# Kernel optimization log

Hardware: AMD Instinct MI355X
Metric: run time of the kernel (lower is better)

## Reference

```python
import jax, jax.numpy as jnp
import numpy as np

BATCH, T, N_STATE, N_IN, N_OUT = 256, 4096, 32, 8, 8
DT = 1e-3


def setup_inputs() -> dict:
    key = jax.random.key(0)
    k_u, k_x0, k_A, k_B, k_C, k_D = jax.random.split(key, 6)
    t = jnp.arange(T, dtype=jnp.float32) * DT
    u = jax.random.normal(k_u, (BATCH, T, N_IN), dtype=jnp.float32)
    x0 = jax.random.normal(k_x0, (BATCH, N_STATE), dtype=jnp.float32)
    # Stable-ish LTI system parameters
    A = (0.1 / np.sqrt(N_STATE)) * jax.random.normal(k_A, (N_STATE, N_STATE), dtype=jnp.float32) - 0.5 * jnp.eye(N_STATE, dtype=jnp.float32)
    B = jax.random.normal(k_B, (N_STATE, N_IN), dtype=jnp.float32) / np.sqrt(N_IN)
    C = jax.random.normal(k_C, (N_OUT, N_STATE), dtype=jnp.float32) / np.sqrt(N_STATE)
    D = jax.random.normal(k_D, (N_OUT, N_IN), dtype=jnp.float32) / np.sqrt(N_IN)
    return {"t": t, "u": u, "x0": x0, "A": A, "B": B, "C": C, "D": D}


def _dopri5_solve(t, u, x0, A, B):
    """Fixed-step Dopri5 (Dormand-Prince 5th order) on a uniform grid.

    Mirrors diffrax.diffeqsolve(Dopri5, ConstantStepSize, dt0=t[1], saveat=ts=t):
    one RK step per grid interval. u is evaluated at stage times via linear
    interpolation between grid samples.
    """
    dt = t[1] - t[0]

    def f(x, uu):  # vector field: dx = A x + B u
        return x @ A.T + uu @ B.T

    ut = jnp.swapaxes(u, 0, 1)  # [T, BATCH, N_IN]

    def step(x, uu):
        u0, u1 = uu
        du = u1 - u0
        k1 = f(x, u0)
        k2 = f(x + dt * (0.2 * k1), u0 + 0.2 * du)
        k3 = f(x + dt * (3.0 / 40.0 * k1 + 9.0 / 40.0 * k2), u0 + 0.3 * du)
        k4 = f(x + dt * (44.0 / 45.0 * k1 - 56.0 / 15.0 * k2 + 32.0 / 9.0 * k3), u0 + 0.8 * du)
        k5 = f(x + dt * (19372.0 / 6561.0 * k1 - 25360.0 / 2187.0 * k2 + 64448.0 / 6561.0 * k3 - 212.0 / 729.0 * k4), u0 + (8.0 / 9.0) * du)
        k6 = f(x + dt * (9017.0 / 3168.0 * k1 - 355.0 / 33.0 * k2 + 46732.0 / 5247.0 * k3 + 49.0 / 176.0 * k4 - 5103.0 / 18656.0 * k5), u1)
        xn = x + dt * (35.0 / 384.0 * k1 + 500.0 / 1113.0 * k3 + 125.0 / 192.0 * k4 - 2187.0 / 6784.0 * k5 + 11.0 / 84.0 * k6)
        return xn, xn

    _, xs_rest = jax.lax.scan(step, x0, (ut[:-1], ut[1:]))
    xs = jnp.concatenate([x0[None], xs_rest], axis=0)  # [T, BATCH, N_STATE]
    return jnp.swapaxes(xs, 0, 1)  # [BATCH, T, N_STATE]


def reference(t, u, x0, A, B, C, D):
    xs = _dopri5_solve(t, u, x0, A, B)          # state trajectory [BATCH, T, N_STATE]
    ys = xs @ C.T + u @ D.T                      # output y = C x + D u, [BATCH, T, N_OUT]
    return xs, ys
```

## Files before the change

### kernel.cpp

```cpp
#include <hip/hip_runtime.h>

#define BATCH 256
#define TT 4096
#define NS 32
#define NI 8
#define NO 8
#define LCH 64
#define NCHUNKS 64

#define WS_M  0
#define WS_N0 1024
#define WS_N1 1280
#define WS_ML 1536
#define WS_V  2560
#define WS_S  (2560 + BATCH * NCHUNKS * NS)
#define WS_F  (WS_S + BATCH * NCHUNKS * NS)

__device__ __forceinline__ float dot4(float4 a, float4 b) {
    return a.x * b.x + a.y * b.y + a.z * b.z + a.w * b.w;
}
__device__ __forceinline__ float4 ld4(const float* p) { return *(const float4*)p; }

__global__ __launch_bounds__(256) void k_pre(const float* __restrict__ tarr,
                                             const float* __restrict__ A,
                                             const float* __restrict__ B,
                                             float* __restrict__ ws) {
    __shared__ float sA[NS * NS], sB[NS * NI];
    __shared__ float Ka[6][NS * NS];
    __shared__ float Kb[6][NS * NI];
    __shared__ float Kc[6][NS * NI];
    __shared__ float Sa[NS * NS], Sb[NS * NI], Sc[NS * NI];
    __shared__ float Pq[2][NS * NS];
    __shared__ float Ms[NS * NS];

    const int tid = threadIdx.x;
    const float dt = tarr[1] - tarr[0];

    for (int e = tid; e < NS * NS; e += 256) sA[e] = A[e];
    for (int e = tid; e < NS * NI; e += 256) sB[e] = B[e];
    __syncthreads();
    for (int e = tid; e < NS * NS; e += 256) Ka[0][e] = sA[e];
    for (int e = tid; e < NS * NI; e += 256) { Kb[0][e] = sB[e]; Kc[0][e] = 0.f; }
    __syncthreads();

    const float atab[5][5] = {
        {0.2f, 0.f, 0.f, 0.f, 0.f},
        {3.f / 40.f, 9.f / 40.f, 0.f, 0.f, 0.f},
        {44.f / 45.f, -56.f / 15.f, 32.f / 9.f, 0.f, 0.f},
        {19372.f / 6561.f, -25360.f / 2187.f, 64448.f / 6561.f, -212.f / 729.f, 0.f},
        {9017.f / 3168.f, -355.f / 33.f, 46732.f / 5247.f, 49.f / 176.f, -5103.f / 18656.f}};
    const float ctab[6] = {0.f, 0.2f, 0.3f, 0.8f, 8.f / 9.f, 1.f};

    for (int st = 1; st <= 5; ++st) {
        for (int e = tid; e < NS * NS; e += 256) {
            float acc = 0.f;
            for (int j = 0; j < st; ++j) acc += atab[st - 1][j] * Ka[j][e];
            Sa[e] = acc;
        }
        for (int e = tid; e < NS * NI; e += 256) {
            float ab = 0.f, ac = 0.f;
            for (int j = 0; j < st; ++j) {
                ab += atab[st - 1][j] * Kb[j][e];
                ac += atab[st - 1][j] * Kc[j][e];
            }
            Sb[e] = ab; Sc[e] = ac;
        }
        __syncthreads();
        {
            const int j = tid & 31, ig = tid >> 5;
            for (int r = 0; r < 4; ++r) {
                const int row = ig + 8 * r;
                float acc = 0.f;
                for (int k = 0; k < NS; ++k) acc += sA[row * NS + k] * Sa[k * NS + j];
                Ka[st][row * NS + j] = sA[row * NS + j] + dt * acc;
            }
            const int jb = tid & 7, rb = tid >> 3;
            float ab = 0.f, ac = 0.f;
            for (int k = 0; k < NS; ++k) {
                ab += sA[rb * NS + k] * Sb[k * NI + jb];
                ac += sA[rb * NS + k] * Sc[k * NI + jb];
            }
            Kb[st][rb * NI + jb] = sB[rb * NI + jb] + dt * ab;
            Kc[st][rb * NI + jb] = ctab[st] * sB[rb * NI + jb] + dt * ac;
        }
        __syncthreads();
    }

    const float btab[6] = {35.f / 384.f, 0.f, 500.f / 1113.f, 125.f / 192.f,
                           -2187.f / 6784.f, 11.f / 84.f};
    for (int e = tid; e < NS * NS; e += 256) {
        float acc = 0.f;
        for (int i2 = 0; i2 < 6; ++i2) acc += btab[i2] * Ka[i2][e];
        const float m = dt * acc + (((e / NS) == (e % NS)) ? 1.f : 0.f);
        ws[WS_M + e] = m;
        Pq[0][e] = m;
        Ms[e] = m;
    }
    for (int e = tid; e < NS * NI; e += 256) {
        float ap = 0.f, aq = 0.f;
        for (int i2 = 0; i2 < 6; ++i2) {
            ap += btab[i2] * Kb[i2][e];
            aq += btab[i2] * Kc[i2][e];
        }
        const float P = dt * ap, Q = dt * aq;
        ws[WS_N0 + e] = P - Q;
        ws[WS_N1 + e] = Q;
        Sb[e] = P - Q;
        Sc[e] = Q;
    }
    __syncthreads();

    int cur = 0;
    for (int itq = 0; itq < 6; ++itq) {
        const int j = tid & 31, ig = tid >> 5;
        for (int r = 0; r < 4; ++r) {
            const int row = ig + 8 * r;
            float acc = 0.f;
            for (int k = 0; k < NS; ++k) acc += Pq[cur][row * NS + k] * Pq[cur][k * NS + j];
            Pq[cur ^ 1][row * NS + j] = acc;
        }
        __syncthreads();
        cur ^= 1;
        if (itq == 2)
            for (int e = tid; e < NS * NS; e += 256) Sa[e] = Pq[cur][e];
    }
    for (int e = tid; e < NS * NS; e += 256) ws[WS_ML + e] = Pq[cur][e];

    float* cb = &Ka[0][0];
    const int rr = tid >> 3, mm = tid & 7;

    float mrow[NS], m8row[NS];
#pragma unroll
    for (int kk = 0; kk < NS; ++kk) { mrow[kk] = Ms[rr * NS + kk]; m8row[kk] = Sa[rr * NS + kk]; }

    {
        float acc = 0.f;
#pragma unroll
        for (int kk = 0; kk < NS; ++kk) acc += mrow[kk] * Sc[kk * NI + mm];
        const float h = Sb[tid] + acc;
        cb[tid] = h;
        ws[WS_F + 63 * (NS * NI) + tid] = h;
    }
    __syncthreads();
    for (int i = 1; i < 8; ++i) {
        float acc = 0.f;
#pragma unroll
        for (int kk = 0; kk < NS; ++kk) acc += m8row[kk] * cb[(i - 1) * 256 + kk * NI + mm];
        cb[i * 256 + tid] = acc;
        ws[WS_F + (63 - 8 * i) * (NS * NI) + tid] = acc;
        __syncthreads();
    }
    int pp = 0;
    for (int k = 1; k < 8; ++k) {
        float acc[8];
#pragma unroll
        for (int i = 0; i < 8; ++i) {
            float a = 0.f;
#pragma unroll
            for (int kk = 0; kk < NS; ++kk) a += mrow[kk] * cb[pp * 2048 + i * 256 + kk * NI + mm];
            acc[i] = a;
        }
#pragma unroll
        for (int i = 0; i < 8; ++i) {
            cb[(pp ^ 1) * 2048 + i * 256 + tid] = acc[i];
            ws[WS_F + (63 - 8 * i - k) * (NS * NI) + tid] = acc[i];
        }
        __syncthreads();
        pp ^= 1;
    }
    ws[WS_F + 64 * (NS * NI) + tid] = Sc[tid];
}

__global__ __launch_bounds__(256, 2) void k_phase1(const float* __restrict__ u,
                                                   float* __restrict__ ws) {
    __shared__ float4 sF[64 * 64];

    const int tid = threadIdx.x;

    const float4* Fg = (const float4*)(ws + WS_F);
    for (int idx = tid; idx < 64 * 64; idx += 256) {
        const int j = idx >> 6, q = (idx >> 3) & 7, s = idx & 7;
        sF[idx] = Fg[(j << 6) + (s << 3) + q];
    }
    __syncthreads();

    const int task = blockIdx.x * 4 + (tid >> 6);
    const int c = task % (NCHUNKS - 1), g = task / (NCHUNKS - 1);
    const int l = tid & 63;
    const int beta = l >> 3, s8 = l & 7;
    const int b = g * 8 + beta;
    const int t0 = c * LCH;
    const float* ub = u + ((size_t)b * TT + t0) * NI;

    float4 ua = ld4(ub), uc = ld4(ub + 4);
    float a0 = 0.f, a1 = 0.f, a2 = 0.f, a3 = 0.f;

#pragma unroll 4
    for (int j = 0; j < 64; ++j) {
        const float4 na = ld4(ub + (j + 1) * NI);
        const float4 nb = ld4(ub + (j + 1) * NI + 4);
        const float4* fj = &sF[(j << 6) + s8];
        const float4 f0 = fj[0], f1 = fj[8], f2 = fj[16], f3 = fj[24];
        const float4 f4 = fj[32], f5 = fj[40], f6 = fj[48], f7 = fj[56];
        a0 += dot4(f0, ua) + dot4(f1, uc);
        a1 += dot4(f2, ua) + dot4(f3, uc);
        a2 += dot4(f4, ua) + dot4(f5, uc);
        a3 += dot4(f6, ua) + dot4(f7, uc);
        ua = na; uc = nb;
    }

    const float* Ft = ws + WS_F + 64 * (NS * NI) + 32 * s8;
    a0 += dot4(ld4(Ft), ua) + dot4(ld4(Ft + 4), uc);
    a1 += dot4(ld4(Ft + 8), ua) + dot4(ld4(Ft + 12), uc);
    a2 += dot4(ld4(Ft + 16), ua) + dot4(ld4(Ft + 20), uc);
    a3 += dot4(ld4(Ft + 24), ua) + dot4(ld4(Ft + 28), uc);

    *(float4*)(ws + WS_V + ((size_t)b * NCHUNKS + c) * NS + 4 * s8) =
        make_float4(a0, a1, a2, a3);
}

__global__ __launch_bounds__(64) void k_phase2(const float* __restrict__ x0,
                                               float* __restrict__ ws) {
    const float* ML = ws + WS_ML;
    const float* v = ws + WS_V;
    float* sst = ws + WS_S;
    const int b = blockIdx.x;
    const int l = threadIdx.x, i = l & 31, h = l >> 5;

    float mlr[16];
#pragma unroll
    for (int jj = 0; jj < 16; ++jj) mlr[jj] = ML[i * NS + 16 * h + jj];

    float x = x0[b * NS + i];
    for (int c = 0; c < NCHUNKS; ++c) {
        if (h == 0) sst[((size_t)b * NCHUNKS + c) * NS + i] = x;
        if (c == NCHUNKS - 1) break;
        float p = 0.f;
#pragma unroll
        for (int jj = 0; jj < 16; ++jj) p += mlr[jj] * __shfl(x, 16 * h + jj, 64);
        p += __shfl_xor(p, 32, 64);
        x = p + v[((size_t)b * NCHUNKS + c) * NS + i];
    }
}

__global__ __launch_bounds__(64, 1) void k_phase3(const float* __restrict__ u,
                                                  float* __restrict__ ws,
                                                  float* __restrict__ out,
                                                  const float* __restrict__ Cc,
                                                  const float* __restrict__ Dd) {
    const float* M = ws + WS_M;
    const float* N0 = ws + WS_N0;
    const float* N1 = ws + WS_N1;

    const int task = blockIdx.x;
    const int c = task % NCHUNKS, g = task / NCHUNKS;
    const int l = threadIdx.x;
    const int beta = l >> 3, s8 = l & 7;
    const int b = g * 8 + beta;

    float4 mq[4][8];
#pragma unroll
    for (int r = 0; r < 4; ++r)
#pragma unroll
        for (int jj = 0; jj < 8; ++jj) mq[r][jj] = ld4(M + (4 * s8 + r) * NS + 4 * jj);

    float4 n0q[4][2], n1q[4][2];
#pragma unroll
    for (int r = 0; r < 4; ++r) {
        n0q[r][0] = ld4(N0 + (4 * s8 + r) * NI);
        n0q[r][1] = ld4(N0 + (4 * s8 + r) * NI + 4);
        n1q[r][0] = ld4(N1 + (4 * s8 + r) * NI);
        n1q[r][1] = ld4(N1 + (4 * s8 + r) * NI + 4);
    }

    float4 cq[8], dq[2];
#pragma unroll
    for (int jj = 0; jj < 8; ++jj) cq[jj] = ld4(Cc + s8 * NS + 4 * jj);
    dq[0] = ld4(Dd + s8 * NI);
    dq[1] = ld4(Dd + s8 * NI + 4);

    __shared__ float4 xb[2][8 * 9];

    const int t0 = c * LCH;
    const float* ub = u + (size_t)b * TT * NI;
    float4 u0a = ld4(ub + t0 * NI), u0b = ld4(ub + t0 * NI + 4);
    float4 u1a = ld4(ub + (t0 + 1) * NI), u1b = ld4(ub + (t0 + 1) * NI + 4);

    float4 mine = ld4(ws + WS_S + ((size_t)b * NCHUNKS + c) * NS + 4 * s8);
    xb[0][beta * 9 + s8] = mine;
    asm volatile("s_waitcnt lgkmcnt(0)" ::: "memory");
    __builtin_amdgcn_sched_barrier(0);

    float* yout = out + (size_t)BATCH * TT * NS;
    int cur = 0;
    for (int js = 0; js < LCH; ++js) {
        const int t = t0 + js;
        float4 xq[8];
#pragma unroll
        for (int jj = 0; jj < 8; ++jj) xq[jj] = xb[cur][beta * 9 + jj];

        const int tp = (t + 2 < TT - 1) ? (t + 2) : (TT - 1);
        const float4 u2a = ld4(ub + tp * NI);
        const float4 u2b = ld4(ub + tp * NI + 4);

        *(float4*)(out + ((size_t)b * TT + t) * NS + 4 * s8) = mine;
        float yv = 0.f;
#pragma unroll
        for (int jj = 0; jj < 8; ++jj) yv += dot4(cq[jj], xq[jj]);
        yv += dot4(dq[0], u0a) + dot4(dq[1], u0b);
        yout[((size_t)b * TT + t) * NO + s8] = yv;

        if (js < LCH - 1) {
            float w0 = dot4(n0q[0][0], u0a) + dot4(n0q[0][1], u0b) + dot4(n1q[0][0], u1a) + dot4(n1q[0][1], u1b);
            float w1 = dot4(n0q[1][0], u0a) + dot4(n0q[1][1], u0b) + dot4(n1q[1][0], u1a) + dot4(n1q[1][1], u1b);
            float w2 = dot4(n0q[2][0], u0a) + dot4(n0q[2][1], u0b) + dot4(n1q[2][0], u1a) + dot4(n1q[2][1], u1b);
            float w3 = dot4(n0q[3][0], u0a) + dot4(n0q[3][1], u0b) + dot4(n1q[3][0], u1a) + dot4(n1q[3][1], u1b);
#pragma unroll
            for (int jj = 0; jj < 8; ++jj) {
                const float4 xv = xq[jj];
                w0 += dot4(mq[0][jj], xv);
                w1 += dot4(mq[1][jj], xv);
                w2 += dot4(mq[2][jj], xv);
                w3 += dot4(mq[3][jj], xv);
            }
            mine = make_float4(w0, w1, w2, w3);
            xb[cur ^ 1][beta * 9 + s8] = mine;
            u0a = u1a; u0b = u1b;
            u1a = u2a; u1b = u2b;
        }
        asm volatile("s_waitcnt lgkmcnt(0)" ::: "memory");
        __builtin_amdgcn_sched_barrier(0);
        cur ^= 1;
    }
}

extern "C" void kernel_launch(void* const* d_in, const int* in_sizes, int n_in,
                              void* d_out, int out_size, void* d_ws, size_t ws_size,
                              hipStream_t stream) {
    const float* t = (const float*)d_in[0];
    const float* u = (const float*)d_in[1];
    const float* x0 = (const float*)d_in[2];
    const float* A = (const float*)d_in[3];
    const float* B = (const float*)d_in[4];
    const float* C = (const float*)d_in[5];
    const float* D = (const float*)d_in[6];
    float* out = (float*)d_out;
    float* ws = (float*)d_ws;

    k_pre<<<dim3(1), dim3(256), 0, stream>>>(t, A, B, ws);
    k_phase1<<<dim3(8 * (NCHUNKS - 1)), dim3(256), 0, stream>>>(u, ws);
    k_phase2<<<dim3(BATCH), dim3(64), 0, stream>>>(x0, ws);
    k_phase3<<<dim3(32 * NCHUNKS), dim3(64), 0, stream>>>(u, ws, out, C, D);
}
```

Baseline: 342.0 us.

## Replace LDS state exchange with wavefront shuffles in phase-3 recurrence

The per-step state broadcast in k_phase3 used to go through a double-buffered shared-memory array with explicit lgkmcnt waits and scheduling barriers. It now uses cross-lane __shfl reads inside the single 64-lane wavefront. The change also splits the dot-product accumulations into independent partial sums to shorten dependency chains, and switches to incrementing pointers for the x, y and u accesses. Shuffles on AMD still go through the LDS crossbar (ds_bpermute), so each step now does 32 shuffles instead of 8 float4 LDS reads, which may cost as much as it saves.

```diff
diff --git a/kernel.cpp b/kernel.cpp
--- a/kernel.cpp
+++ b/kernel.cpp
@@ -257,6 +257,7 @@
     const int l = threadIdx.x;
     const int beta = l >> 3, s8 = l & 7;
     const int b = g * 8 + beta;
+    const int src_base = l & 56;
 
     float4 mq[4][8];
 #pragma unroll
@@ -279,58 +280,61 @@
     dq[0] = ld4(Dd + s8 * NI);
     dq[1] = ld4(Dd + s8 * NI + 4);
 
-    __shared__ float4 xb[2][8 * 9];
-
     const int t0 = c * LCH;
     const float* ub = u + (size_t)b * TT * NI;
-    float4 u0a = ld4(ub + t0 * NI), u0b = ld4(ub + t0 * NI + 4);
-    float4 u1a = ld4(ub + (t0 + 1) * NI), u1b = ld4(ub + (t0 + 1) * NI + 4);
+    const float* u_last = ub + (size_t)(TT - 1) * NI;
+    const float* up = ub + (size_t)t0 * NI;
+    float4 u0a = ld4(up), u0b = ld4(up + 4);
+    float4 u1a = ld4(up + NI), u1b = ld4(up + NI + 4);
+    const float* up2 = up + 2 * NI;
 
     float4 mine = ld4(ws + WS_S + ((size_t)b * NCHUNKS + c) * NS + 4 * s8);
-    xb[0][beta * 9 + s8] = mine;
-    asm volatile("s_waitcnt lgkmcnt(0)" ::: "memory");
-    __builtin_amdgcn_sched_barrier(0);
-
-    float* yout = out + (size_t)BATCH * TT * NS;
-    int cur = 0;
+
+    float* xp = out + ((size_t)b * TT + t0) * NS + 4 * s8;
+    float* yp = out + (size_t)BATCH * TT * NS + ((size_t)b * TT + t0) * NO + s8;
+
     for (int js = 0; js < LCH; ++js) {
-        const int t = t0 + js;
         float4 xq[8];
 #pragma unroll
-        for (int jj = 0; jj < 8; ++jj) xq[jj] = xb[cur][beta * 9 + jj];
-
-        const int tp = (t + 2 < TT - 1) ? (t + 2) : (TT - 1);
-        const float4 u2a = ld4(ub + tp * NI);
-        const float4 u2b = ld4(ub + tp * NI + 4);
-
-        *(float4*)(out + ((size_t)b * TT + t) * NS + 4 * s8) = mine;
-        float yv = 0.f;
-#pragma unroll
-        for (int jj = 0; jj < 8; ++jj) yv += dot4(cq[jj], xq[jj]);
-        yv += dot4(dq[0], u0a) + dot4(dq[1], u0b);
-        yout[((size_t)b * TT + t) * NO + s8] = yv;
+        for (int jj = 0; jj < 8; ++jj) {
+            xq[jj].x = __shfl(mine.x, src_base + jj, 64);
+            xq[jj].y = __shfl(mine.y, src_base + jj, 64);
+            xq[jj].z = __shfl(mine.z, src_base + jj, 64);
+            xq[jj].w = __shfl(mine.w, src_base + jj, 64);
+        }
+
+        const float* uq = (up2 > u_last) ? u_last : up2;
+        const float4 u2a = ld4(uq);
+        const float4 u2b = ld4(uq + 4);
+
+        *(float4*)xp = mine;
+
+        float ya = dot4(cq[0], xq[0]) + dot4(cq[1], xq[1]) + dot4(cq[2], xq[2]) + dot4(cq[3], xq[3]);
+        float yb = dot4(cq[4], xq[4]) + dot4(cq[5], xq[5]) + dot4(cq[6], xq[6]) + dot4(cq[7], xq[7]);
+        ya += dot4(dq[0], u0a);
+        yb += dot4(dq[1], u0b);
+        *yp = ya + yb;
 
         if (js < LCH - 1) {
-            float w0 = dot4(n0q[0][0], u0a) + dot4(n0q[0][1], u0b) + dot4(n1q[0][0], u1a) + dot4(n1q[0][1], u1b);
-            float w1 = dot4(n0q[1][0], u0a) + dot4(n0q[1][1], u0b) + dot4(n1q[1][0], u1a) + dot4(n1q[1][1], u1b);
-            float w2 = dot4(n0q[2][0], u0a) + dot4(n0q[2][1], u0b) + dot4(n1q[2][0], u1a) + dot4(n1q[2][1], u1b);
-            float w3 = dot4(n0q[3][0], u0a) + dot4(n0q[3][1], u0b) + dot4(n1q[3][0], u1a) + dot4(n1q[3][1], u1b);
-#pragma unroll
-            for (int jj = 0; jj < 8; ++jj) {
-                const float4 xv = xq[jj];
-                w0 += dot4(mq[0][jj], xv);
-                w1 += dot4(mq[1][jj], xv);
-                w2 += dot4(mq[2][jj], xv);
-                w3 += dot4(mq[3][jj], xv);
+            float w0, w1, w2, w3;
+#pragma unroll
+            for (int r = 0; r < 4; ++r) {
+                const float pn = dot4(n0q[r][0], u0a) + dot4(n0q[r][1], u0b) +
+                                 dot4(n1q[r][0], u1a) + dot4(n1q[r][1], u1b);
+                const float pe = dot4(mq[r][0], xq[0]) + dot4(mq[r][2], xq[2]) +
+                                 dot4(mq[r][4], xq[4]) + dot4(mq[r][6], xq[6]);
+                const float po = dot4(mq[r][1], xq[1]) + dot4(mq[r][3], xq[3]) +
+                                 dot4(mq[r][5], xq[5]) + dot4(mq[r][7], xq[7]);
+                const float w = pn + pe + po;
+                if (r == 0) w0 = w; else if (r == 1) w1 = w; else if (r == 2) w2 = w; else w3 = w;
             }
             mine = make_float4(w0, w1, w2, w3);
-            xb[cur ^ 1][beta * 9 + s8] = mine;
             u0a = u1a; u0b = u1b;
             u1a = u2a; u1b = u2b;
         }
-        asm volatile("s_waitcnt lgkmcnt(0)" ::: "memory");
-        __builtin_amdgcn_sched_barrier(0);
-        cur ^= 1;
+        xp += NS;
+        yp += NO;
+        up2 += NI;
     }
 }
 
```

Result: slower. 380.6 us (+11.3%).
